# Kernel optimization log

Measured on AMD Instinct MI355X. Metric: run time of the kernel, lower is better.

The kernel has to match this reference:

```python
import jax, jax.numpy as jnp
import numpy as np

NUM_ITERATIONS = 3


def _squash(s):
    # Faithful to the torch code: squash over dim=2 of s_j [B,1,nu,us,1],
    # which is the num_units axis. In our [B, nu, us] layout that is axis=1.
    mag_sq = jnp.sum(s ** 2, axis=1, keepdims=True)  # [B,1,us]
    mag = jnp.sqrt(mag_sq)
    return mag_sq / (1.0 + mag_sq) * (s / mag)


def setup_inputs() -> dict:
    key = jax.random.key(0)
    k1, k2 = jax.random.split(key)
    B, in_units, in_channels, num_units, unit_size = 256, 8, 1152, 10, 16
    x = jax.random.normal(k1, (B, in_units, in_channels), dtype=jnp.float32)
    W = jax.random.normal(k2, (1, in_channels, num_units, unit_size, in_units), dtype=jnp.float32)
    return {"x": x, "W": W}


def reference(x, W):
    B = x.shape[0]
    W0 = W[0]  # [ic, nu, us, iu]
    ic, nu = W0.shape[0], W0.shape[1]
    xt = jnp.swapaxes(x, 1, 2)  # [B, ic, iu]
    # u_hat = W @ x per (batch, in_channel, out_unit): [B, ic, nu, us]
    u_hat = jnp.einsum('cdui,bci->bcdu', W0, xt)
    b_ij = jnp.zeros((ic, nu), dtype=x.dtype)
    v = None
    for _ in range(NUM_ITERATIONS):
        c_ij = jax.nn.softmax(b_ij, axis=0)              # softmax over in_channels
        s_j = jnp.einsum('cd,bcdu->bdu', c_ij, u_hat)    # [B, nu, us]
        v = _squash(s_j)                                 # [B, nu, us]
        # agreement: <u_hat, v> over unit_size, mean over batch -> [ic, nu]
        agree = jnp.einsum('bcdu,bdu->cd', u_hat, v) / B
        b_ij = b_ij + agree
    return v  # [B, num_units, unit_size]
```

## Files before the change

kernel.cpp:

```cpp
#include <hip/hip_runtime.h>
#include <math.h>

#define B   256
#define IU  8
#define IC  1152
#define NU  10
#define US  16
#define ROWS (B * IU)

__global__ __launch_bounds__(256) void transpose_x(const float* __restrict__ x,
                                                   float* __restrict__ xT) {
    __shared__ float t[32][33];
    const int tx = threadIdx.x & 31, ty = threadIdx.x >> 5;
    const int ct = blockIdx.x % 36;
    const int rt = blockIdx.x / 36;
    const int c0 = ct * 32, r0 = rt * 32;
#pragma unroll
    for (int k = 0; k < 32; k += 8)
        t[ty + k][tx] = x[(size_t)(r0 + ty + k) * IC + c0 + tx];
    __syncthreads();
#pragma unroll
    for (int k = 0; k < 32; k += 8)
        xT[(size_t)(c0 + ty + k) * ROWS + r0 + tx] = t[tx][ty + k];
}

#define CCH 9
#define NCH 128
#define BT  64

__global__ __launch_bounds__(256) void s_pass(const float* __restrict__ xT,
                                              const float* __restrict__ W,
                                              const float* __restrict__ cT,
                                              float* __restrict__ sp) {
    __shared__ float4 ws[CCH * NU * 2 * 16];
    __shared__ __align__(16) float xs[CCH * BT * IU];
    __shared__ float cs[NU * CCH];
    const int tid = threadIdx.x;
    const int bt = blockIdx.x & 3;
    const int ch = blockIdx.x >> 2;
    const int b0 = bt * BT, c0 = ch * CCH;

    const float4* wg = (const float4*)W + (size_t)c0 * 320;
    for (int q = tid; q < CCH * NU * 32; q += 256) {
        int h = q & 1, u = (q >> 1) & 15, cd = q >> 5;
        ws[(cd * 2 + h) * 16 + u] = wg[q];
    }
    const float4* xg = (const float4*)xT;
    float4* xsv = (float4*)xs;
    for (int q = tid; q < CCH * BT * 2; q += 256) {
        int cc = q >> 7, r = q & 127;
        xsv[cc * 128 + r] = xg[(size_t)(c0 + cc) * (ROWS / 4) + b0 * 2 + r];
    }
    float scale;
    if (cT) {
        for (int q = tid; q < NU * CCH; q += 256)
            cs[q] = cT[(q / CCH) * IC + c0 + (q % CCH)];
        scale = 1.0f;
    } else {
        for (int q = tid; q < NU * CCH; q += 256) cs[q] = 1.0f;
        scale = 1.0f / (float)IC;
    }
    __syncthreads();

    const int uq = tid & 15;
    const int bs = tid >> 4;

    float acc[4][NU];
#pragma unroll
    for (int bb = 0; bb < 4; bb++)
#pragma unroll
        for (int d = 0; d < NU; d++) acc[bb][d] = 0.0f;

#pragma unroll 3
    for (int cc = 0; cc < CCH; cc++) {
        float4 xv0[4], xv1[4];
#pragma unroll
        for (int bb = 0; bb < 4; bb++) {
            const float4* xp = (const float4*)(xs + (cc * BT + bs + 16 * bb) * IU);
            xv0[bb] = xp[0]; xv1[bb] = xp[1];
        }
#pragma unroll
        for (int d = 0; d < NU; d++) {
            const float cw = cs[d * CCH + cc];
            float4 w0 = ws[((cc * NU + d) * 2 + 0) * 16 + uq];
            float4 w1 = ws[((cc * NU + d) * 2 + 1) * 16 + uq];
#pragma unroll
            for (int bb = 0; bb < 4; bb++) {
                float uh = w0.x * xv0[bb].x + w0.y * xv0[bb].y + w0.z * xv0[bb].z + w0.w * xv0[bb].w
                         + w1.x * xv1[bb].x + w1.y * xv1[bb].y + w1.z * xv1[bb].z + w1.w * xv1[bb].w;
                acc[bb][d] = fmaf(cw, uh, acc[bb][d]);
            }
        }
    }
#pragma unroll
    for (int bb = 0; bb < 4; bb++) {
        const int b = b0 + bs + 16 * bb;
#pragma unroll
        for (int d = 0; d < NU; d++)
            sp[(((size_t)ch * B + b) * NU + d) * US + uq] = acc[bb][d] * scale;
    }
}

__global__ __launch_bounds__(192) void squash_k(const float* __restrict__ sp,
                                                float* __restrict__ vout) {
    __shared__ float smag[NU * US];
    const int b = blockIdx.x;
    const int tid = threadIdx.x;
    const int d = tid >> 4, uq = tid & 15;
    float s = 0.0f;
    if (d < NU) {
#pragma unroll 8
        for (int chp = 0; chp < NCH; chp++)
            s += sp[(((size_t)chp * B + b) * NU + d) * US + uq];
        smag[d * US + uq] = s * s;
    }
    __syncthreads();
    if (d < NU) {
        float msq = 0.0f;
#pragma unroll
        for (int dd = 0; dd < NU; dd++) msq += smag[dd * US + uq];
        float f = msq / ((1.0f + msq) * sqrtf(msq));
        vout[((size_t)b * NU + d) * US + uq] = s * f;
    }
}

#define ACT 16
#define ABT 32
#define NBCH 8

__global__ __launch_bounds__(256) void agree_k(const float* __restrict__ xT,
                                               const float* __restrict__ W,
                                               const float* __restrict__ v,
                                               float* __restrict__ ap) {
    __shared__ __align__(16) float xs[ABT * 132];
    __shared__ __align__(16) float vs[ABT * NU * US];
    const int tid = threadIdx.x;
    const int ct = blockIdx.x % 72;
    const int bch = blockIdx.x / 72;
    const int c0 = ct * ACT, b0 = bch * ABT;
    const int uq = tid & 15, cl = tid >> 4;

    const float4* wg = (const float4*)W + (size_t)(c0 + cl) * 320 + uq * 2;
    float4 wA[NU], wB[NU];
#pragma unroll
    for (int d = 0; d < NU; d++) { wA[d] = wg[d * 32]; wB[d] = wg[d * 32 + 1]; }

    const float4* xg = (const float4*)xT;
    for (int q = tid; q < ACT * ABT * 2; q += 256) {
        int h = q & 1, bl = (q >> 1) & 31, cc = q >> 6;
        float4 val = xg[(size_t)(c0 + cc) * (ROWS / 4) + (b0 + bl) * 2 + h];
        *(float4*)(xs + bl * 132 + cc * 8 + h * 4) = val;
    }
    const float4* vg = (const float4*)(v + (size_t)b0 * NU * US);
    float4* vsv = (float4*)vs;
    for (int q = tid; q < ABT * NU * US / 4; q += 256)
        vsv[q] = vg[q];
    __syncthreads();

    float acc[NU];
#pragma unroll
    for (int d = 0; d < NU; d++) acc[d] = 0.0f;

#pragma unroll 4
    for (int bl = 0; bl < ABT; bl++) {
        const float4* xp = (const float4*)(xs + bl * 132 + cl * 8);
        float4 x0 = xp[0], x1 = xp[1];
        const float* vp = vs + bl * NU * US + uq;
#pragma unroll
        for (int d = 0; d < NU; d++) {
            float uh = wA[d].x * x0.x + wA[d].y * x0.y + wA[d].z * x0.z + wA[d].w * x0.w
                     + wB[d].x * x1.x + wB[d].y * x1.y + wB[d].z * x1.z + wB[d].w * x1.w;
            acc[d] = fmaf(uh, vp[d * 16], acc[d]);
        }
    }
#pragma unroll
    for (int d = 0; d < NU; d++) {
        float a = acc[d];
        a += __shfl_xor(a, 1, 64);
        a += __shfl_xor(a, 2, 64);
        a += __shfl_xor(a, 4, 64);
        a += __shfl_xor(a, 8, 64);
        if (uq == 0)
            ap[((size_t)bch * NU + d) * IC + c0 + cl] = a;
    }
}

__global__ __launch_bounds__(384) void bsm_k(const float* __restrict__ ap,
                                             float* __restrict__ bij,
                                             float* __restrict__ cT,
                                             int first) {
    __shared__ float wred[8];
    __shared__ float bcast;
    const int d = blockIdx.x;
    const int tid = threadIdx.x;
    float bn[3];
    float lmax = -1e30f;
#pragma unroll
    for (int k = 0; k < 3; k++) {
        int c = tid + k * 384;
        float a = 0.0f;
#pragma unroll
        for (int g = 0; g < NBCH; g++) a += ap[((size_t)g * NU + d) * IC + c];
        a *= (1.0f / (float)B);
        float bo = first ? 0.0f : bij[d * IC + c];
        bn[k] = bo + a;
        bij[d * IC + c] = bn[k];
        lmax = fmaxf(lmax, bn[k]);
    }
    for (int off = 32; off > 0; off >>= 1) lmax = fmaxf(lmax, __shfl_down(lmax, off, 64));
    const int wid = tid >> 6, lane = tid & 63;
    if (lane == 0) wred[wid] = lmax;
    __syncthreads();
    if (tid == 0) {
        float m = wred[0];
        for (int w_ = 1; w_ < 6; w_++) m = fmaxf(m, wred[w_]);
        bcast = m;
    }
    __syncthreads();
    const float mx = bcast;
    float e[3];
    float lsum = 0.0f;
#pragma unroll
    for (int k = 0; k < 3; k++) { e[k] = expf(bn[k] - mx); lsum += e[k]; }
    for (int off = 32; off > 0; off >>= 1) lsum += __shfl_down(lsum, off, 64);
    if (lane == 0) wred[wid] = lsum;
    __syncthreads();
    if (tid == 0) {
        float s2 = 0.0f;
        for (int w_ = 0; w_ < 6; w_++) s2 += wred[w_];
        bcast = 1.0f / s2;
    }
    __syncthreads();
    const float inv = bcast;
#pragma unroll
    for (int k = 0; k < 3; k++) cT[d * IC + tid + k * 384] = e[k] * inv;
}

extern "C" void kernel_launch(void* const* d_in, const int* in_sizes, int n_in,
                              void* d_out, int out_size, void* d_ws, size_t ws_size,
                              hipStream_t stream) {
    (void)in_sizes; (void)n_in; (void)out_size; (void)ws_size;
    const float* x = (const float*)d_in[0];
    const float* W = (const float*)d_in[1];
    float* out = (float*)d_out;

    float* xT  = (float*)d_ws;
    float* sp  = xT + (size_t)IC * ROWS;
    float* v   = sp + (size_t)NCH * B * NU * US;
    float* bij = v + (size_t)B * NU * US;
    float* cTb = bij + (size_t)NU * IC;
    float* apg = cTb + (size_t)NU * IC;

    transpose_x<<<36 * 64, 256, 0, stream>>>(x, xT);

    s_pass<<<512, 256, 0, stream>>>(xT, W, nullptr, sp);
    squash_k<<<B, 192, 0, stream>>>(sp, v);
    agree_k<<<72 * NBCH, 256, 0, stream>>>(xT, W, v, apg);
    bsm_k<<<NU, 384, 0, stream>>>(apg, bij, cTb, 1);
    s_pass<<<512, 256, 0, stream>>>(xT, W, cTb, sp);
    squash_k<<<B, 192, 0, stream>>>(sp, v);
    agree_k<<<72 * NBCH, 256, 0, stream>>>(xT, W, v, apg);
    bsm_k<<<NU, 384, 0, stream>>>(apg, bij, cTb, 0);
    s_pass<<<512, 256, 0, stream>>>(xT, W, cTb, sp);
    squash_k<<<B, 192, 0, stream>>>(sp, out);
}
```

Before: 200.6 us.

## Fold routing coefficients into shared W and remap blocks for XCD locality

In the s_pass kernel, the routing coefficient c is now multiplied into the W tile while it is staged into shared memory. The inner loop then becomes a plain fma chain with no per-element coefficient multiply and no separate shared c array. Both s_pass and agree_k now remap blockIdx so that blocks sharing the same channel tile land on the same XCD, improving L2 reuse of W and xT on MI355X's chiplet layout. The fma chain changes rounding order slightly, and the remap assumes the block count is a multiple of the XCD grouping.

```diff
diff --git a/kernel.cpp b/kernel.cpp
--- a/kernel.cpp
+++ b/kernel.cpp
@@ -34,16 +34,27 @@
                                               float* __restrict__ sp) {
     __shared__ float4 ws[CCH * NU * 2 * 16];
     __shared__ __align__(16) float xs[CCH * BT * IU];
-    __shared__ float cs[NU * CCH];
-    const int tid = threadIdx.x;
-    const int bt = blockIdx.x & 3;
-    const int ch = blockIdx.x >> 2;
+    const int tid = threadIdx.x;
+    const int xcd  = blockIdx.x & 7;
+    const int slot = blockIdx.x >> 3;
+    const int ch   = ((slot >> 2) << 3) | xcd;
+    const int bt   = slot & 3;
     const int b0 = bt * BT, c0 = ch * CCH;
 
     const float4* wg = (const float4*)W + (size_t)c0 * 320;
-    for (int q = tid; q < CCH * NU * 32; q += 256) {
-        int h = q & 1, u = (q >> 1) & 15, cd = q >> 5;
-        ws[(cd * 2 + h) * 16 + u] = wg[q];
+    if (cT) {
+        for (int q = tid; q < CCH * NU * 32; q += 256) {
+            int h = q & 1, u = (q >> 1) & 15, cd = q >> 5;
+            int cc = cd / 10, d = cd - cc * 10;
+            float cw = cT[d * IC + c0 + cc];
+            float4 wv = wg[q];
+            ws[(cd * 2 + h) * 16 + u] = make_float4(wv.x * cw, wv.y * cw, wv.z * cw, wv.w * cw);
+        }
+    } else {
+        for (int q = tid; q < CCH * NU * 32; q += 256) {
+            int h = q & 1, u = (q >> 1) & 15, cd = q >> 5;
+            ws[(cd * 2 + h) * 16 + u] = wg[q];
+        }
     }
     const float4* xg = (const float4*)xT;
     float4* xsv = (float4*)xs;
@@ -51,15 +62,7 @@
         int cc = q >> 7, r = q & 127;
         xsv[cc * 128 + r] = xg[(size_t)(c0 + cc) * (ROWS / 4) + b0 * 2 + r];
     }
-    float scale;
-    if (cT) {
-        for (int q = tid; q < NU * CCH; q += 256)
-            cs[q] = cT[(q / CCH) * IC + c0 + (q % CCH)];
-        scale = 1.0f;
-    } else {
-        for (int q = tid; q < NU * CCH; q += 256) cs[q] = 1.0f;
-        scale = 1.0f / (float)IC;
-    }
+    const float scale = cT ? 1.0f : (1.0f / (float)IC);
     __syncthreads();
 
     const int uq = tid & 15;
@@ -81,14 +84,20 @@
         }
 #pragma unroll
         for (int d = 0; d < NU; d++) {
-            const float cw = cs[d * CCH + cc];
             float4 w0 = ws[((cc * NU + d) * 2 + 0) * 16 + uq];
             float4 w1 = ws[((cc * NU + d) * 2 + 1) * 16 + uq];
 #pragma unroll
             for (int bb = 0; bb < 4; bb++) {
-                float uh = w0.x * xv0[bb].x + w0.y * xv0[bb].y + w0.z * xv0[bb].z + w0.w * xv0[bb].w
-                         + w1.x * xv1[bb].x + w1.y * xv1[bb].y + w1.z * xv1[bb].z + w1.w * xv1[bb].w;
-                acc[bb][d] = fmaf(cw, uh, acc[bb][d]);
+                float a = acc[bb][d];
+                a = fmaf(w0.x, xv0[bb].x, a);
+                a = fmaf(w0.y, xv0[bb].y, a);
+                a = fmaf(w0.z, xv0[bb].z, a);
+                a = fmaf(w0.w, xv0[bb].w, a);
+                a = fmaf(w1.x, xv1[bb].x, a);
+                a = fmaf(w1.y, xv1[bb].y, a);
+                a = fmaf(w1.z, xv1[bb].z, a);
+                a = fmaf(w1.w, xv1[bb].w, a);
+                acc[bb][d] = a;
             }
         }
     }
@@ -135,8 +144,10 @@
     __shared__ __align__(16) float xs[ABT * 132];
     __shared__ __align__(16) float vs[ABT * NU * US];
     const int tid = threadIdx.x;
-    const int ct = blockIdx.x % 72;
-    const int bch = blockIdx.x / 72;
+    const int xcd  = blockIdx.x & 7;
+    const int slot = blockIdx.x >> 3;
+    const int ct   = ((slot >> 3) << 3) | xcd;
+    const int bch  = slot & 7;
     const int c0 = ct * ACT, b0 = bch * ABT;
     const int uq = tid & 15, cl = tid >> 4;
 
```

New measurement: 200.9 us. Within noise of the previous version (+0.1%).

## Fuse routing iterations into one persistent kernel with software grid barriers

Applied to the files above, without the earlier changes.

Replaces the ten separate s_pass/squash/agree/softmax launches with a single persistent 512-block kernel that keeps W and x tiles resident in LDS across all three routing iterations. Phases are separated by a hierarchical atomic grid barrier, and the agreement step reuses the on-chip tiles instead of reloading W and x from global memory. The softmax state b_ij is held in registers of the first ten blocks. It removes launch gaps and repeated global loads, but it relies on all 512 blocks being co-resident (two per CU). It also adds spin-wait barrier latency and leaves only a few blocks doing the serial squash and softmax phases.

```diff
diff --git a/kernel.cpp b/kernel.cpp
--- a/kernel.cpp
+++ b/kernel.cpp
@@ -1,12 +1,16 @@
 #include <hip/hip_runtime.h>
 #include <math.h>
 
-#define B   256
+#define B_  256
 #define IU  8
 #define IC  1152
 #define NU  10
 #define US  16
-#define ROWS (B * IU)
+#define ROWS 2048
+#define CCH 9
+#define NCH 128
+#define BT  64
+#define NBLK 512
 
 __global__ __launch_bounds__(256) void transpose_x(const float* __restrict__ x,
                                                    float* __restrict__ xT) {
@@ -24,20 +28,52 @@
         xT[(size_t)(c0 + ty + k) * ROWS + r0 + tx] = t[tx][ty + k];
 }
 
-#define CCH 9
-#define NCH 128
-#define BT  64
-
-__global__ __launch_bounds__(256) void s_pass(const float* __restrict__ xT,
-                                              const float* __restrict__ W,
-                                              const float* __restrict__ cT,
-                                              float* __restrict__ sp) {
+__device__ __forceinline__ void gridbar(unsigned* bar, int grp) {
+    __syncthreads();
+    if (threadIdx.x == 0) {
+        __threadfence();
+        unsigned* gen = bar + 144;
+        unsigned g = __hip_atomic_load(gen, __ATOMIC_RELAXED, __HIP_MEMORY_SCOPE_AGENT);
+        unsigned a = __hip_atomic_fetch_add(bar + grp * 16, 1u, __ATOMIC_ACQ_REL,
+                                            __HIP_MEMORY_SCOPE_AGENT);
+        if (a == (NBLK / 8 - 1)) {
+            __hip_atomic_store(bar + grp * 16, 0u, __ATOMIC_RELAXED, __HIP_MEMORY_SCOPE_AGENT);
+            unsigned r = __hip_atomic_fetch_add(bar + 128, 1u, __ATOMIC_ACQ_REL,
+                                                __HIP_MEMORY_SCOPE_AGENT);
+            if (r == 7u) {
+                __hip_atomic_store(bar + 128, 0u, __ATOMIC_RELAXED, __HIP_MEMORY_SCOPE_AGENT);
+                __hip_atomic_store(gen, g + 1u, __ATOMIC_RELEASE, __HIP_MEMORY_SCOPE_AGENT);
+            } else {
+                while (__hip_atomic_load(gen, __ATOMIC_RELAXED, __HIP_MEMORY_SCOPE_AGENT) == g)
+                    __builtin_amdgcn_s_sleep(2);
+            }
+        } else {
+            while (__hip_atomic_load(gen, __ATOMIC_RELAXED, __HIP_MEMORY_SCOPE_AGENT) == g)
+                __builtin_amdgcn_s_sleep(2);
+        }
+        __threadfence();
+    }
+    __syncthreads();
+}
+
+__global__ __launch_bounds__(256, 2) void mega(const float* __restrict__ xT,
+                                               const float* __restrict__ W,
+                                               float* __restrict__ sp,
+                                               float* __restrict__ vbuf,
+                                               float* __restrict__ ap,
+                                               float* __restrict__ cT,
+                                               float* __restrict__ out,
+                                               unsigned* __restrict__ bar) {
     __shared__ float4 ws[CCH * NU * 2 * 16];
     __shared__ __align__(16) float xs[CCH * BT * IU];
-    __shared__ float cs[NU * CCH];
+    __shared__ float scratch[168];
+
     const int tid = threadIdx.x;
-    const int bt = blockIdx.x & 3;
-    const int ch = blockIdx.x >> 2;
+    const int bid = blockIdx.x;
+    const int grp = bid & 7;
+    const int slot = bid >> 3;
+    const int ch = ((slot >> 2) << 3) | grp;
+    const int bt = slot & 3;
     const int b0 = bt * BT, c0 = ch * CCH;
 
     const float4* wg = (const float4*)W + (size_t)c0 * 320;
@@ -51,189 +87,167 @@
         int cc = q >> 7, r = q & 127;
         xsv[cc * 128 + r] = xg[(size_t)(c0 + cc) * (ROWS / 4) + b0 * 2 + r];
     }
-    float scale;
-    if (cT) {
-        for (int q = tid; q < NU * CCH; q += 256)
-            cs[q] = cT[(q / CCH) * IC + c0 + (q % CCH)];
-        scale = 1.0f;
-    } else {
-        for (int q = tid; q < NU * CCH; q += 256) cs[q] = 1.0f;
-        scale = 1.0f / (float)IC;
-    }
-    __syncthreads();
 
     const int uq = tid & 15;
     const int bs = tid >> 4;
-
-    float acc[4][NU];
-#pragma unroll
-    for (int bb = 0; bb < 4; bb++)
-#pragma unroll
-        for (int d = 0; d < NU; d++) acc[bb][d] = 0.0f;
+    float bn[5] = {0.f, 0.f, 0.f, 0.f, 0.f};
+
+    for (int iter = 0; iter < 3; ++iter) {
+        __syncthreads();
+        if (iter == 0) {
+            for (int q = tid; q < NU * CCH; q += 256) scratch[q] = 1.0f;
+        } else {
+            for (int q = tid; q < NU * CCH; q += 256) {
+                int d = q / CCH, cc = q - d * CCH;
+                scratch[q] = cT[d * IC + c0 + cc];
+            }
+        }
+        __syncthreads();
+        const float scale = iter ? 1.0f : (1.0f / (float)IC);
+
+        {
+            float acc[4][NU];
+#pragma unroll
+            for (int bb = 0; bb < 4; bb++)
+#pragma unroll
+                for (int d = 0; d < NU; d++) acc[bb][d] = 0.0f;
 
 #pragma unroll 3
-    for (int cc = 0; cc < CCH; cc++) {
-        float4 xv0[4], xv1[4];
-#pragma unroll
-        for (int bb = 0; bb < 4; bb++) {
-            const float4* xp = (const float4*)(xs + (cc * BT + bs + 16 * bb) * IU);
-            xv0[bb] = xp[0]; xv1[bb] = xp[1];
-        }
-#pragma unroll
-        for (int d = 0; d < NU; d++) {
-            const float cw = cs[d * CCH + cc];
-            float4 w0 = ws[((cc * NU + d) * 2 + 0) * 16 + uq];
-            float4 w1 = ws[((cc * NU + d) * 2 + 1) * 16 + uq];
+            for (int cc = 0; cc < CCH; cc++) {
+                float4 xv0[4], xv1[4];
+#pragma unroll
+                for (int bb = 0; bb < 4; bb++) {
+                    const float4* xp = (const float4*)(xs + (cc * BT + bs + 16 * bb) * IU);
+                    xv0[bb] = xp[0]; xv1[bb] = xp[1];
+                }
+#pragma unroll
+                for (int d = 0; d < NU; d++) {
+                    float4 w0 = ws[((cc * NU + d) * 2 + 0) * 16 + uq];
+                    float4 w1 = ws[((cc * NU + d) * 2 + 1) * 16 + uq];
+                    const float cw = scratch[d * CCH + cc];
+#pragma unroll
+                    for (int bb = 0; bb < 4; bb++) {
+                        float uh = w0.x * xv0[bb].x + w0.y * xv0[bb].y + w0.z * xv0[bb].z + w0.w * xv0[bb].w
+                                 + w1.x * xv1[bb].x + w1.y * xv1[bb].y + w1.z * xv1[bb].z + w1.w * xv1[bb].w;
+                        acc[bb][d] = fmaf(cw, uh, acc[bb][d]);
+                    }
+                }
+            }
 #pragma unroll
             for (int bb = 0; bb < 4; bb++) {
-                float uh = w0.x * xv0[bb].x + w0.y * xv0[bb].y + w0.z * xv0[bb].z + w0.w * xv0[bb].w
-                         + w1.x * xv1[bb].x + w1.y * xv1[bb].y + w1.z * xv1[bb].z + w1.w * xv1[bb].w;
-                acc[bb][d] = fmaf(cw, uh, acc[bb][d]);
-            }
-        }
-    }
-#pragma unroll
-    for (int bb = 0; bb < 4; bb++) {
-        const int b = b0 + bs + 16 * bb;
-#pragma unroll
-        for (int d = 0; d < NU; d++)
-            sp[(((size_t)ch * B + b) * NU + d) * US + uq] = acc[bb][d] * scale;
-    }
-}
-
-__global__ __launch_bounds__(192) void squash_k(const float* __restrict__ sp,
-                                                float* __restrict__ vout) {
-    __shared__ float smag[NU * US];
-    const int b = blockIdx.x;
-    const int tid = threadIdx.x;
-    const int d = tid >> 4, uq = tid & 15;
-    float s = 0.0f;
-    if (d < NU) {
+                const int b = b0 + bs + 16 * bb;
+#pragma unroll
+                for (int d = 0; d < NU; d++)
+                    sp[(((size_t)ch * B_ + b) * NU + d) * US + uq] = acc[bb][d] * scale;
+            }
+        }
+        gridbar(bar, grp);
+
+        if (bid < B_) {
+            const int d = tid >> 4;
+            float s = 0.0f;
+            if (tid < NU * US) {
 #pragma unroll 8
-        for (int chp = 0; chp < NCH; chp++)
-            s += sp[(((size_t)chp * B + b) * NU + d) * US + uq];
-        smag[d * US + uq] = s * s;
-    }
-    __syncthreads();
-    if (d < NU) {
-        float msq = 0.0f;
-#pragma unroll
-        for (int dd = 0; dd < NU; dd++) msq += smag[dd * US + uq];
-        float f = msq / ((1.0f + msq) * sqrtf(msq));
-        vout[((size_t)b * NU + d) * US + uq] = s * f;
-    }
-}
-
-#define ACT 16
-#define ABT 32
-#define NBCH 8
-
-__global__ __launch_bounds__(256) void agree_k(const float* __restrict__ xT,
-                                               const float* __restrict__ W,
-                                               const float* __restrict__ v,
-                                               float* __restrict__ ap) {
-    __shared__ __align__(16) float xs[ABT * 132];
-    __shared__ __align__(16) float vs[ABT * NU * US];
-    const int tid = threadIdx.x;
-    const int ct = blockIdx.x % 72;
-    const int bch = blockIdx.x / 72;
-    const int c0 = ct * ACT, b0 = bch * ABT;
-    const int uq = tid & 15, cl = tid >> 4;
-
-    const float4* wg = (const float4*)W + (size_t)(c0 + cl) * 320 + uq * 2;
-    float4 wA[NU], wB[NU];
-#pragma unroll
-    for (int d = 0; d < NU; d++) { wA[d] = wg[d * 32]; wB[d] = wg[d * 32 + 1]; }
-
-    const float4* xg = (const float4*)xT;
-    for (int q = tid; q < ACT * ABT * 2; q += 256) {
-        int h = q & 1, bl = (q >> 1) & 31, cc = q >> 6;
-        float4 val = xg[(size_t)(c0 + cc) * (ROWS / 4) + (b0 + bl) * 2 + h];
-        *(float4*)(xs + bl * 132 + cc * 8 + h * 4) = val;
-    }
-    const float4* vg = (const float4*)(v + (size_t)b0 * NU * US);
-    float4* vsv = (float4*)vs;
-    for (int q = tid; q < ABT * NU * US / 4; q += 256)
-        vsv[q] = vg[q];
-    __syncthreads();
-
-    float acc[NU];
-#pragma unroll
-    for (int d = 0; d < NU; d++) acc[d] = 0.0f;
-
+                for (int chp = 0; chp < NCH; chp++)
+                    s += sp[(((size_t)chp * B_ + bid) * NU + d) * US + uq];
+                scratch[tid] = s * s;
+            }
+            __syncthreads();
+            if (tid < NU * US) {
+                float msq = 0.0f;
+#pragma unroll
+                for (int dd = 0; dd < NU; dd++) msq += scratch[dd * US + uq];
+                float f = msq / ((1.0f + msq) * sqrtf(msq));
+                float* dst = (iter == 2) ? out : vbuf;
+                dst[((size_t)bid * NU + d) * US + uq] = s * f;
+            }
+        }
+        if (iter == 2) return;
+        gridbar(bar, grp);
+
+        {
+            const int cl = tid >> 4;
+            if (cl < CCH) {
+                float4 wA[NU], wB[NU];
+#pragma unroll
+                for (int d = 0; d < NU; d++) {
+                    wA[d] = ws[((cl * NU + d) * 2 + 0) * 16 + uq];
+                    wB[d] = ws[((cl * NU + d) * 2 + 1) * 16 + uq];
+                }
+                float accd[NU];
+#pragma unroll
+                for (int d = 0; d < NU; d++) accd[d] = 0.0f;
+                const int bstag = (cl & 3) * 7;
 #pragma unroll 4
-    for (int bl = 0; bl < ABT; bl++) {
-        const float4* xp = (const float4*)(xs + bl * 132 + cl * 8);
-        float4 x0 = xp[0], x1 = xp[1];
-        const float* vp = vs + bl * NU * US + uq;
-#pragma unroll
-        for (int d = 0; d < NU; d++) {
-            float uh = wA[d].x * x0.x + wA[d].y * x0.y + wA[d].z * x0.z + wA[d].w * x0.w
-                     + wB[d].x * x1.x + wB[d].y * x1.y + wB[d].z * x1.z + wB[d].w * x1.w;
-            acc[d] = fmaf(uh, vp[d * 16], acc[d]);
-        }
-    }
-#pragma unroll
-    for (int d = 0; d < NU; d++) {
-        float a = acc[d];
-        a += __shfl_xor(a, 1, 64);
-        a += __shfl_xor(a, 2, 64);
-        a += __shfl_xor(a, 4, 64);
-        a += __shfl_xor(a, 8, 64);
-        if (uq == 0)
-            ap[((size_t)bch * NU + d) * IC + c0 + cl] = a;
-    }
-}
-
-__global__ __launch_bounds__(384) void bsm_k(const float* __restrict__ ap,
-                                             float* __restrict__ bij,
-                                             float* __restrict__ cT,
-                                             int first) {
-    __shared__ float wred[8];
-    __shared__ float bcast;
-    const int d = blockIdx.x;
-    const int tid = threadIdx.x;
-    float bn[3];
-    float lmax = -1e30f;
-#pragma unroll
-    for (int k = 0; k < 3; k++) {
-        int c = tid + k * 384;
-        float a = 0.0f;
-#pragma unroll
-        for (int g = 0; g < NBCH; g++) a += ap[((size_t)g * NU + d) * IC + c];
-        a *= (1.0f / (float)B);
-        float bo = first ? 0.0f : bij[d * IC + c];
-        bn[k] = bo + a;
-        bij[d * IC + c] = bn[k];
-        lmax = fmaxf(lmax, bn[k]);
-    }
-    for (int off = 32; off > 0; off >>= 1) lmax = fmaxf(lmax, __shfl_down(lmax, off, 64));
-    const int wid = tid >> 6, lane = tid & 63;
-    if (lane == 0) wred[wid] = lmax;
-    __syncthreads();
-    if (tid == 0) {
-        float m = wred[0];
-        for (int w_ = 1; w_ < 6; w_++) m = fmaxf(m, wred[w_]);
-        bcast = m;
-    }
-    __syncthreads();
-    const float mx = bcast;
-    float e[3];
-    float lsum = 0.0f;
-#pragma unroll
-    for (int k = 0; k < 3; k++) { e[k] = expf(bn[k] - mx); lsum += e[k]; }
-    for (int off = 32; off > 0; off >>= 1) lsum += __shfl_down(lsum, off, 64);
-    if (lane == 0) wred[wid] = lsum;
-    __syncthreads();
-    if (tid == 0) {
-        float s2 = 0.0f;
-        for (int w_ = 0; w_ < 6; w_++) s2 += wred[w_];
-        bcast = 1.0f / s2;
-    }
-    __syncthreads();
-    const float inv = bcast;
-#pragma unroll
-    for (int k = 0; k < 3; k++) cT[d * IC + tid + k * 384] = e[k] * inv;
+                for (int blx = 0; blx < BT; blx++) {
+                    const int bl = (blx + bstag) & 63;
+                    const float* xp = xs + (cl * BT + bl) * IU;
+                    float4 x0 = *(const float4*)xp;
+                    float4 x1 = *(const float4*)(xp + 4);
+                    const float* vp = vbuf + (size_t)(b0 + bl) * NU * US + uq;
+#pragma unroll
+                    for (int d = 0; d < NU; d++) {
+                        float uh = wA[d].x * x0.x + wA[d].y * x0.y + wA[d].z * x0.z + wA[d].w * x0.w
+                                 + wB[d].x * x1.x + wB[d].y * x1.y + wB[d].z * x1.z + wB[d].w * x1.w;
+                        accd[d] = fmaf(uh, vp[d * US], accd[d]);
+                    }
+                }
+#pragma unroll
+                for (int d = 0; d < NU; d++) {
+                    float a = accd[d];
+                    a += __shfl_xor(a, 1, 64);
+                    a += __shfl_xor(a, 2, 64);
+                    a += __shfl_xor(a, 4, 64);
+                    a += __shfl_xor(a, 8, 64);
+                    if (uq == 0) ap[((size_t)bt * NU + d) * IC + c0 + cl] = a;
+                }
+            }
+        }
+        gridbar(bar, grp);
+
+        if (bid < NU) {
+            const int d = bid;
+            float lmax = -1e30f;
+#pragma unroll
+            for (int k = 0; k < 5; k++) {
+                int c = tid + k * 256;
+                if (c < IC) {
+                    float a = 0.0f;
+#pragma unroll
+                    for (int g = 0; g < 4; g++) a += ap[((size_t)g * NU + d) * IC + c];
+                    bn[k] += a * (1.0f / (float)B_);
+                    lmax = fmaxf(lmax, bn[k]);
+                }
+            }
+            for (int off = 32; off > 0; off >>= 1) lmax = fmaxf(lmax, __shfl_down(lmax, off, 64));
+            const int wid = tid >> 6, lane = tid & 63;
+            if (lane == 0) scratch[wid] = lmax;
+            __syncthreads();
+            if (tid == 0)
+                scratch[8] = fmaxf(fmaxf(scratch[0], scratch[1]), fmaxf(scratch[2], scratch[3]));
+            __syncthreads();
+            const float mx = scratch[8];
+            float e[5];
+            float lsum = 0.0f;
+#pragma unroll
+            for (int k = 0; k < 5; k++) {
+                int c = tid + k * 256;
+                if (c < IC) { e[k] = expf(bn[k] - mx); lsum += e[k]; }
+            }
+            for (int off = 32; off > 0; off >>= 1) lsum += __shfl_down(lsum, off, 64);
+            if (lane == 0) scratch[wid] = lsum;
+            __syncthreads();
+            if (tid == 0) scratch[8] = 1.0f / (scratch[0] + scratch[1] + scratch[2] + scratch[3]);
+            __syncthreads();
+            const float inv = scratch[8];
+#pragma unroll
+            for (int k = 0; k < 5; k++) {
+                int c = tid + k * 256;
+                if (c < IC) cT[d * IC + c] = e[k] * inv;
+            }
+        }
+        gridbar(bar, grp);
+    }
 }
 
 extern "C" void kernel_launch(void* const* d_in, const int* in_sizes, int n_in,
@@ -244,23 +258,14 @@
     const float* W = (const float*)d_in[1];
     float* out = (float*)d_out;
 
-    float* xT  = (float*)d_ws;
+    unsigned* bar = (unsigned*)d_ws;
+    float* xT  = (float*)d_ws + 256;
     float* sp  = xT + (size_t)IC * ROWS;
-    float* v   = sp + (size_t)NCH * B * NU * US;
-    float* bij = v + (size_t)B * NU * US;
-    float* cTb = bij + (size_t)NU * IC;
+    float* v   = sp + (size_t)NCH * B_ * NU * US;
+    float* cTb = v + (size_t)B_ * NU * US;
     float* apg = cTb + (size_t)NU * IC;
 
+    hipMemsetAsync(d_ws, 0, 1024, stream);
     transpose_x<<<36 * 64, 256, 0, stream>>>(x, xT);
-
-    s_pass<<<512, 256, 0, stream>>>(xT, W, nullptr, sp);
-    squash_k<<<B, 192, 0, stream>>>(sp, v);
-    agree_k<<<72 * NBCH, 256, 0, stream>>>(xT, W, v, apg);
-    bsm_k<<<NU, 384, 0, stream>>>(apg, bij, cTb, 1);
-    s_pass<<<512, 256, 0, stream>>>(xT, W, cTb, sp);
-    squash_k<<<B, 192, 0, stream>>>(sp, v);
-    agree_k<<<72 * NBCH, 256, 0, stream>>>(xT, W, v, apg);
-    bsm_k<<<NU, 384, 0, stream>>>(apg, bij, cTb, 0);
-    s_pass<<<512, 256, 0, stream>>>(xT, W, cTb, sp);
-    squash_k<<<B, 192, 0, stream>>>(sp, out);
-}
+    mega<<<NBLK, 256, 0, stream>>>(xT, W, sp, v, apg, cTb, out, bar);
+}
```

After: 491.1 us. 145% more time.
